# Optimization experiments

Measured on AMD Instinct MI355X. Metric: run time of the kernel, lower is better.

## Reference

```python
import jax, jax.numpy as jnp
import numpy as np

SIGMA = 20.0  # outlier threshold used by FindOutliers
EPS = 1e-8


def setup_inputs() -> dict:
    key = jax.random.key(0)
    k1, k2, k3 = jax.random.split(key, 3)
    B, S, K, N = 2, 2048, 4096, 4096
    x = jax.random.normal(k1, (B, S, K), jnp.float32)
    # inject 8 outlier feature columns (|x| > sigma) so the fp correction path is exercised
    out_cols = jnp.arange(8) * (K // 8)
    x = x.at[:, :, out_cols].multiply(30.0)
    weight = jax.random.normal(k2, (N, K), jnp.float32) * (1.0 / np.sqrt(K))
    bias = jax.random.normal(k3, (N,), jnp.float32) * 0.01
    return {"x": x, "weight": weight, "bias": bias}


def reference(x, weight, bias):
    # x: [B,S,K], weight: [N,K], bias: [N]
    B, S, K = x.shape
    N = weight.shape[0]
    xf = x.reshape(-1, K)  # [M,K]

    # FindOutliers: columns where any activation exceeds sigma (as a fixed-size mask)
    col_mask = jnp.any(jnp.abs(xf) > SIGMA, axis=0)          # [K] bool
    keep = jnp.logical_not(col_mask)

    # weight quantization: zero outlier columns, per-output-row symmetric int8
    w_in = weight * keep[None, :].astype(weight.dtype)        # [N,K]
    q_scale = jnp.max(jnp.abs(w_in), axis=1) / 127.0          # [N]
    q_scale = jnp.maximum(q_scale, EPS)
    q_w = jnp.round(jnp.clip(w_in / q_scale[:, None], -128.0, 127.0)).astype(jnp.int8)

    # per-token (row) activation quantization (FindRowScaleF32)
    row_scale = jnp.max(jnp.abs(xf), axis=1, keepdims=True) / 127.0  # [M,1] fp32
    row_scale = jnp.maximum(row_scale, EPS)
    q_x = jnp.round(jnp.clip(xf / row_scale, -128.0, 127.0)).astype(jnp.int8)

    # int8 GEMM with int32 accumulation, then dequant + bias
    acc = jnp.matmul(q_x.astype(jnp.int32), q_w.T.astype(jnp.int32)).astype(jnp.float32)  # [M,N]
    y = acc * row_scale * q_scale[None, :]

    # fp outlier correction: x[:, ind] @ weight[:, ind].T  (dense masked form, same math)
    x_out = xf * col_mask[None, :].astype(xf.dtype)
    y = y + x_out @ weight.T

    y = y + bias[None, :]
    return y.reshape(B, S, N)
```

## Files before the change

### kernel.cpp

```cpp
#include <hip/hip_runtime.h>
#include <stdint.h>

#define K_DIM 4096
#define N_DIM 4096
#define SIGMA 20.0f
#define EPSQ 1e-8f

typedef __attribute__((ext_vector_type(4))) int i32x4;

#define GLDS16(gp, lp)                                                         \
  __builtin_amdgcn_global_load_lds(                                            \
      (const __attribute__((address_space(1))) unsigned int*)(const void*)(gp),\
      (__attribute__((address_space(3))) unsigned int*)(void*)(lp), 16, 0, 0)

__global__ __launch_bounds__(256) void k_rowquant(
    const float* __restrict__ x, float* __restrict__ row_scale,
    int* __restrict__ mask, int8_t* __restrict__ qx)
{
  const int m = blockIdx.x;
  const int t = threadIdx.x;
  const float4* xr = (const float4*)(x + (size_t)m * K_DIM);
  float4 v[4];
  float amax = 0.0f;
#pragma unroll
  for (int i = 0; i < 4; ++i) {
    v[i] = xr[t + i * 256];
    float a0 = fabsf(v[i].x), a1 = fabsf(v[i].y);
    float a2 = fabsf(v[i].z), a3 = fabsf(v[i].w);
    amax = fmaxf(amax, fmaxf(fmaxf(a0, a1), fmaxf(a2, a3)));
    int kbase = (t + i * 256) * 4;
    if (a0 > SIGMA) mask[kbase + 0] = 1;
    if (a1 > SIGMA) mask[kbase + 1] = 1;
    if (a2 > SIGMA) mask[kbase + 2] = 1;
    if (a3 > SIGMA) mask[kbase + 3] = 1;
  }
#pragma unroll
  for (int off = 32; off > 0; off >>= 1)
    amax = fmaxf(amax, __shfl_down(amax, off, 64));
  __shared__ float smax[4];
  __shared__ float sscale;
  if ((t & 63) == 0) smax[t >> 6] = amax;
  __syncthreads();
  if (t == 0) {
    float ms = fmaxf(fmaxf(smax[0], smax[1]), fmaxf(smax[2], smax[3]));
    float rs = fmaxf(ms / 127.0f, EPSQ);
    sscale = rs;
    row_scale[m] = rs;
  }
  __syncthreads();
  const float rs = sscale;
  uint32_t* qxo = (uint32_t*)(qx + (size_t)m * K_DIM);
#pragma unroll
  for (int i = 0; i < 4; ++i) {
    int q0 = (int)rintf(fminf(fmaxf(v[i].x / rs, -128.0f), 127.0f));
    int q1 = (int)rintf(fminf(fmaxf(v[i].y / rs, -128.0f), 127.0f));
    int q2 = (int)rintf(fminf(fmaxf(v[i].z / rs, -128.0f), 127.0f));
    int q3 = (int)rintf(fminf(fmaxf(v[i].w / rs, -128.0f), 127.0f));
    uint32_t packed = (uint32_t)(q0 & 0xff) | ((uint32_t)(q1 & 0xff) << 8) |
                      ((uint32_t)(q2 & 0xff) << 16) | ((uint32_t)(q3 & 0xff) << 24);
    qxo[t + i * 256] = packed;
  }
}

__global__ __launch_bounds__(256) void k_compact(
    const int* __restrict__ mask, int* __restrict__ outlist,
    int* __restrict__ count)
{
  int k = blockIdx.x * 256 + threadIdx.x;
  if (mask[k]) {
    int idx = atomicAdd(count, 1);
    outlist[idx] = k;
  }
}

__global__ __launch_bounds__(256) void k_wquant(
    const float* __restrict__ w, const int* __restrict__ mask,
    float* __restrict__ q_scale, int8_t* __restrict__ qw)
{
  const int n = blockIdx.x;
  const int t = threadIdx.x;
  const float4* wr = (const float4*)(w + (size_t)n * K_DIM);
  const int4* mr = (const int4*)mask;
  float4 v[4];
  float amax = 0.0f;
#pragma unroll
  for (int i = 0; i < 4; ++i) {
    float4 vv = wr[t + i * 256];
    int4 mm = mr[t + i * 256];
    vv.x = mm.x ? 0.0f : vv.x;
    vv.y = mm.y ? 0.0f : vv.y;
    vv.z = mm.z ? 0.0f : vv.z;
    vv.w = mm.w ? 0.0f : vv.w;
    v[i] = vv;
    amax = fmaxf(amax, fmaxf(fmaxf(fabsf(vv.x), fabsf(vv.y)),
                             fmaxf(fabsf(vv.z), fabsf(vv.w))));
  }
#pragma unroll
  for (int off = 32; off > 0; off >>= 1)
    amax = fmaxf(amax, __shfl_down(amax, off, 64));
  __shared__ float smax[4];
  __shared__ float sscale;
  if ((t & 63) == 0) smax[t >> 6] = amax;
  __syncthreads();
  if (t == 0) {
    float ms = fmaxf(fmaxf(smax[0], smax[1]), fmaxf(smax[2], smax[3]));
    float qs = fmaxf(ms / 127.0f, EPSQ);
    sscale = qs;
    q_scale[n] = qs;
  }
  __syncthreads();
  const float qs = sscale;
  uint32_t* qwo = (uint32_t*)(qw + (size_t)n * K_DIM);
#pragma unroll
  for (int i = 0; i < 4; ++i) {
    int q0 = (int)rintf(fminf(fmaxf(v[i].x / qs, -128.0f), 127.0f));
    int q1 = (int)rintf(fminf(fmaxf(v[i].y / qs, -128.0f), 127.0f));
    int q2 = (int)rintf(fminf(fmaxf(v[i].z / qs, -128.0f), 127.0f));
    int q3 = (int)rintf(fminf(fmaxf(v[i].w / qs, -128.0f), 127.0f));
    uint32_t packed = (uint32_t)(q0 & 0xff) | ((uint32_t)(q1 & 0xff) << 8) |
                      ((uint32_t)(q2 & 0xff) << 16) | ((uint32_t)(q3 & 0xff) << 24);
    qwo[t + i * 256] = packed;
  }
}

__global__ __launch_bounds__(256) void k_gemm(
    const int8_t* __restrict__ qx, const int8_t* __restrict__ qw,
    const float* __restrict__ row_scale, const float* __restrict__ q_scale,
    const float* __restrict__ bias,
    const float* __restrict__ x, const float* __restrict__ w,
    const int* __restrict__ outlist, const int* __restrict__ outcount,
    float* __restrict__ out)
{
  __shared__ int8_t As[128 * 64];
  __shared__ int8_t Bs[128 * 64];
  __shared__ float xsh[128][8];
  __shared__ float wsh[128][8];

  const int t = threadIdx.x;
  const int m0 = blockIdx.y * 128;
  const int n0 = blockIdx.x * 128;

  const int lane = t & 63;
  const int wave = t >> 6;
  const int wm = (wave & 1) * 64;
  const int wn = (wave >> 1) * 64;
  const int lrow = lane & 15;
  const int kg = lane >> 4;

  i32x4 acc[4][4] = {};

  const int srow = t >> 2;
  const int clog = (t & 3) ^ ((t >> 3) & 3);
  const int8_t* gA = qx + (size_t)(m0 + srow) * K_DIM + clog * 16;
  const int8_t* gB = qw + (size_t)(n0 + srow) * K_DIM + clog * 16;

  int offA[4], offB[4];
#pragma unroll
  for (int i = 0; i < 4; ++i) {
    int rA = wm + i * 16 + lrow;
    offA[i] = rA * 64 + ((kg ^ ((rA >> 1) & 3)) * 16);
    int rB = wn + i * 16 + lrow;
    offB[i] = rB * 64 + ((kg ^ ((rB >> 1) & 3)) * 16);
  }

  for (int k0 = 0; k0 < K_DIM; k0 += 64) {
    GLDS16(gA + k0,                        As + t * 16);
    GLDS16(gA + (size_t)64 * K_DIM + k0,   As + 4096 + t * 16);
    GLDS16(gB + k0,                        Bs + t * 16);
    GLDS16(gB + (size_t)64 * K_DIM + k0,   Bs + 4096 + t * 16);
    __syncthreads();

    i32x4 af[4], bf[4];
#pragma unroll
    for (int i = 0; i < 4; ++i) af[i] = *(const i32x4*)(As + offA[i]);
#pragma unroll
    for (int j = 0; j < 4; ++j) bf[j] = *(const i32x4*)(Bs + offB[j]);
#pragma unroll
    for (int i = 0; i < 4; ++i)
#pragma unroll
      for (int j = 0; j < 4; ++j)
        acc[i][j] = __builtin_amdgcn_mfma_i32_16x16x64_i8(af[i], bf[j], acc[i][j], 0, 0, 0);
    __syncthreads();
  }

  const int cnt = *outcount;
  const int cs = cnt < 8 ? cnt : 8;
#pragma unroll
  for (int u = 0; u < 4; ++u) {
    int idx = t * 4 + u;
    int rr = idx >> 3;
    int oo = idx & 7;
    float xv = 0.0f, wv = 0.0f;
    if (oo < cs) {
      int kcol = outlist[oo];
      xv = x[(size_t)(m0 + rr) * K_DIM + kcol];
      wv = w[(size_t)(n0 + rr) * K_DIM + kcol];
    }
    xsh[rr][oo] = xv;
    wsh[rr][oo] = wv;
  }
  __syncthreads();

  float qs[4], bv[4];
  int gn[4];
#pragma unroll
  for (int j = 0; j < 4; ++j) {
    gn[j] = n0 + wn + j * 16 + lrow;
    qs[j] = q_scale[gn[j]];
    bv[j] = bias[gn[j]];
  }

#pragma unroll
  for (int i = 0; i < 4; ++i) {
#pragma unroll
    for (int r = 0; r < 4; ++r) {
      int ml = wm + i * 16 + kg * 4 + r;
      int gm = m0 + ml;
      float rs = row_scale[gm];
      float xvv[8];
#pragma unroll
      for (int o = 0; o < 8; ++o) xvv[o] = xsh[ml][o];
#pragma unroll
      for (int j = 0; j < 4; ++j) {
        int nl = wn + j * 16 + lrow;
        float corr = 0.0f;
#pragma unroll
        for (int o = 0; o < 8; ++o) corr += xvv[o] * wsh[nl][o];
        for (int o = 8; o < cnt; ++o)
          corr += x[(size_t)gm * K_DIM + outlist[o]] *
                  w[(size_t)gn[j] * K_DIM + outlist[o]];
        float val = (float)acc[i][j][r] * rs * qs[j] + corr + bv[j];
        out[(size_t)gm * N_DIM + gn[j]] = val;
      }
    }
  }
}

extern "C" void kernel_launch(void* const* d_in, const int* in_sizes, int n_in,
                              void* d_out, int out_size, void* d_ws, size_t ws_size,
                              hipStream_t stream) {
  const float* x = (const float*)d_in[0];
  const float* w = (const float*)d_in[1];
  const float* bias = (const float*)d_in[2];
  float* out = (float*)d_out;
  const int M = in_sizes[0] / K_DIM;

  char* ws = (char*)d_ws;
  int* mask = (int*)(ws);
  int* count = (int*)(ws + 16384);
  int* outlist = (int*)(ws + 20480);
  float* row_scale = (float*)(ws + 36864);
  float* q_scale = (float*)(ws + 53248);
  int8_t* qx = (int8_t*)(ws + 131072);
  int8_t* qw = (int8_t*)(ws + 131072 + (size_t)M * K_DIM);

  hipMemsetAsync(ws, 0, 20480, stream);
  k_rowquant<<<M, 256, 0, stream>>>(x, row_scale, mask, qx);
  k_compact<<<K_DIM / 256, 256, 0, stream>>>(mask, outlist, count);
  k_wquant<<<N_DIM, 256, 0, stream>>>(w, mask, q_scale, qw);
  dim3 grid(N_DIM / 128, M / 128);
  k_gemm<<<grid, dim3(256, 1, 1), 0, stream>>>(qx, qw, row_scale, q_scale, bias,
                                               x, w, outlist, count, out);
}
```

Before: 271.1 us.

## Enlarge int8 GEMM tiles to 256x256 with 4-stage LDS pipeline

Reworks the int8 GEMM kernel to use 512-thread blocks computing 256x256 output tiles. Operands stream into a 4-buffer LDS ring through global_load_lds, with explicit vmcnt waits so up to three k-tiles are in flight. Each k-step is split into two MFMA halves, with the next tile's loads interleaved between them and s_setprio raising priority around the MFMA bursts. The goal is to hide global-load latency and get more operand reuse per LDS byte. The cost is about 128KB of LDS per block and a grid of only 256 blocks, which limits occupancy and load balancing; the outlier staging buffers now reuse the LDS tile space.

```diff
diff --git a/kernel.cpp b/kernel.cpp
--- a/kernel.cpp
+++ b/kernel.cpp
@@ -123,7 +123,7 @@
   }
 }
 
-__global__ __launch_bounds__(256) void k_gemm(
+__global__ __launch_bounds__(512, 2) void k_gemm(
     const int8_t* __restrict__ qx, const int8_t* __restrict__ qw,
     const float* __restrict__ row_scale, const float* __restrict__ q_scale,
     const float* __restrict__ bias,
@@ -131,58 +131,103 @@
     const int* __restrict__ outlist, const int* __restrict__ outcount,
     float* __restrict__ out)
 {
-  __shared__ int8_t As[128 * 64];
-  __shared__ int8_t Bs[128 * 64];
-  __shared__ float xsh[128][8];
-  __shared__ float wsh[128][8];
+  __shared__ int8_t As[4][256 * 64];
+  __shared__ int8_t Bs[4][256 * 64];
 
   const int t = threadIdx.x;
-  const int m0 = blockIdx.y * 128;
-  const int n0 = blockIdx.x * 128;
-
+  const int m0 = blockIdx.y * 256;
+  const int n0 = blockIdx.x * 256;
   const int lane = t & 63;
   const int wave = t >> 6;
-  const int wm = (wave & 1) * 64;
-  const int wn = (wave >> 1) * 64;
+  const int wm = (wave >> 2) * 128;
+  const int wn = (wave & 3) * 64;
   const int lrow = lane & 15;
   const int kg = lane >> 4;
 
-  i32x4 acc[4][4] = {};
+  i32x4 acc[8][4] = {};
 
   const int srow = t >> 2;
-  const int clog = (t & 3) ^ ((t >> 3) & 3);
-  const int8_t* gA = qx + (size_t)(m0 + srow) * K_DIM + clog * 16;
-  const int8_t* gB = qw + (size_t)(n0 + srow) * K_DIM + clog * 16;
-
-  int offA[4], offB[4];
-#pragma unroll
-  for (int i = 0; i < 4; ++i) {
+  const int sclog = (t & 3) ^ ((srow >> 1) & 3);
+  const int8_t* gA = qx + (size_t)(m0 + srow) * K_DIM + sclog * 16;
+  const int8_t* gB = qw + (size_t)(n0 + srow) * K_DIM + sclog * 16;
+
+  int offA[8], offB[4];
+#pragma unroll
+  for (int i = 0; i < 8; ++i) {
     int rA = wm + i * 16 + lrow;
     offA[i] = rA * 64 + ((kg ^ ((rA >> 1) & 3)) * 16);
-    int rB = wn + i * 16 + lrow;
-    offB[i] = rB * 64 + ((kg ^ ((rB >> 1) & 3)) * 16);
-  }
-
-  for (int k0 = 0; k0 < K_DIM; k0 += 64) {
-    GLDS16(gA + k0,                        As + t * 16);
-    GLDS16(gA + (size_t)64 * K_DIM + k0,   As + 4096 + t * 16);
-    GLDS16(gB + k0,                        Bs + t * 16);
-    GLDS16(gB + (size_t)64 * K_DIM + k0,   Bs + 4096 + t * 16);
-    __syncthreads();
+  }
+#pragma unroll
+  for (int j = 0; j < 4; ++j) {
+    int rB = wn + j * 16 + lrow;
+    offB[j] = rB * 64 + ((kg ^ ((rB >> 1) & 3)) * 16);
+  }
+
+#define STAGE_A(b, tt) do {                                                    \
+    GLDS16(gA + (size_t)(tt) * 64, &As[b][t * 16]);                            \
+    GLDS16(gA + (size_t)128 * K_DIM + (size_t)(tt) * 64, &As[b][8192 + t * 16]);\
+  } while (0)
+#define STAGE_B(b, tt) do {                                                    \
+    GLDS16(gB + (size_t)(tt) * 64, &Bs[b][t * 16]);                            \
+    GLDS16(gB + (size_t)128 * K_DIM + (size_t)(tt) * 64, &Bs[b][8192 + t * 16]);\
+  } while (0)
+
+  STAGE_A(0, 0); STAGE_B(0, 0);
+  STAGE_A(1, 1); STAGE_B(1, 1);
+  STAGE_A(2, 2); STAGE_B(2, 2);
+  asm volatile("s_waitcnt vmcnt(8)" ::: "memory");
+  __builtin_amdgcn_s_barrier();
+
+#pragma unroll 4
+  for (int kt = 0; kt < 64; ++kt) {
+    const int cur = kt & 3;
+    const int nx = (kt + 3) & 3;
+    const int ktn = (kt + 3) & 63;
+    const int8_t* a = &As[cur][0];
+    const int8_t* b = &Bs[cur][0];
 
     i32x4 af[4], bf[4];
 #pragma unroll
-    for (int i = 0; i < 4; ++i) af[i] = *(const i32x4*)(As + offA[i]);
-#pragma unroll
-    for (int j = 0; j < 4; ++j) bf[j] = *(const i32x4*)(Bs + offB[j]);
+    for (int i = 0; i < 4; ++i) af[i] = *(const i32x4*)(a + offA[i]);
+#pragma unroll
+    for (int j = 0; j < 4; ++j) bf[j] = *(const i32x4*)(b + offB[j]);
+    STAGE_A(nx, ktn);
+    __builtin_amdgcn_s_barrier();
+    asm volatile("s_waitcnt lgkmcnt(0)" ::: "memory");
+    __builtin_amdgcn_sched_barrier(0);
+    __builtin_amdgcn_s_setprio(1);
 #pragma unroll
     for (int i = 0; i < 4; ++i)
 #pragma unroll
       for (int j = 0; j < 4; ++j)
         acc[i][j] = __builtin_amdgcn_mfma_i32_16x16x64_i8(af[i], bf[j], acc[i][j], 0, 0, 0);
-    __syncthreads();
-  }
-
+    __builtin_amdgcn_s_setprio(0);
+    __builtin_amdgcn_s_barrier();
+
+    i32x4 af2[4];
+#pragma unroll
+    for (int i = 0; i < 4; ++i) af2[i] = *(const i32x4*)(a + offA[4 + i]);
+    STAGE_B(nx, ktn);
+    __builtin_amdgcn_s_barrier();
+    asm volatile("s_waitcnt lgkmcnt(0)" ::: "memory");
+    __builtin_amdgcn_sched_barrier(0);
+    __builtin_amdgcn_s_setprio(1);
+#pragma unroll
+    for (int i = 0; i < 4; ++i)
+#pragma unroll
+      for (int j = 0; j < 4; ++j)
+        acc[4 + i][j] = __builtin_amdgcn_mfma_i32_16x16x64_i8(af2[i], bf[j], acc[4 + i][j], 0, 0, 0);
+    __builtin_amdgcn_s_setprio(0);
+    asm volatile("s_waitcnt vmcnt(8)" ::: "memory");
+    __builtin_amdgcn_s_barrier();
+  }
+
+#undef STAGE_A
+#undef STAGE_B
+
+  __syncthreads();
+  float* xsh = (float*)&As[0][0];
+  float* wsh = (float*)&Bs[0][0];
   const int cnt = *outcount;
   const int cs = cnt < 8 ? cnt : 8;
 #pragma unroll
@@ -196,8 +241,8 @@
       xv = x[(size_t)(m0 + rr) * K_DIM + kcol];
       wv = w[(size_t)(n0 + rr) * K_DIM + kcol];
     }
-    xsh[rr][oo] = xv;
-    wsh[rr][oo] = wv;
+    xsh[rr * 8 + oo] = xv;
+    wsh[rr * 8 + oo] = wv;
   }
   __syncthreads();
 
@@ -211,7 +256,7 @@
   }
 
 #pragma unroll
-  for (int i = 0; i < 4; ++i) {
+  for (int i = 0; i < 8; ++i) {
 #pragma unroll
     for (int r = 0; r < 4; ++r) {
       int ml = wm + i * 16 + kg * 4 + r;
@@ -219,13 +264,13 @@
       float rs = row_scale[gm];
       float xvv[8];
 #pragma unroll
-      for (int o = 0; o < 8; ++o) xvv[o] = xsh[ml][o];
+      for (int o = 0; o < 8; ++o) xvv[o] = xsh[ml * 8 + o];
 #pragma unroll
       for (int j = 0; j < 4; ++j) {
         int nl = wn + j * 16 + lrow;
         float corr = 0.0f;
 #pragma unroll
-        for (int o = 0; o < 8; ++o) corr += xvv[o] * wsh[nl][o];
+        for (int o = 0; o < 8; ++o) corr += xvv[o] * wsh[nl * 8 + o];
         for (int o = 8; o < cnt; ++o)
           corr += x[(size_t)gm * K_DIM + outlist[o]] *
                   w[(size_t)gn[j] * K_DIM + outlist[o]];
@@ -258,7 +303,7 @@
   k_rowquant<<<M, 256, 0, stream>>>(x, row_scale, mask, qx);
   k_compact<<<K_DIM / 256, 256, 0, stream>>>(mask, outlist, count);
   k_wquant<<<N_DIM, 256, 0, stream>>>(w, mask, q_scale, qw);
-  dim3 grid(N_DIM / 128, M / 128);
-  k_gemm<<<grid, dim3(256, 1, 1), 0, stream>>>(qx, qw, row_scale, q_scale, bias,
+  dim3 grid(N_DIM / 256, M / 256);
+  k_gemm<<<grid, dim3(512, 1, 1), 0, stream>>>(qx, qw, row_scale, q_scale, bias,
                                                x, w, outlist, count, out);
 }
```

Result: faster. 248.1 us (-8.5%).
